# Kernel optimization log

Hardware: AMD Instinct MI355X
Metric: run time of the kernel (lower is better)

## Reference

```python
import jax, jax.numpy as jnp
import numpy as np

N_NODES = 100000
N_EDGES = 1600000
D = 128
EPS = 1e-5


def setup_inputs() -> dict:
    key = jax.random.key(0)
    k1, k2, k3 = jax.random.split(key, 3)
    x = jax.random.normal(k1, (N_NODES, D), dtype=jnp.float32)
    edge_index = jax.random.randint(k2, (2, N_EDGES), 0, N_NODES, dtype=jnp.int64)
    W = jax.random.normal(k3, (D, D), dtype=jnp.float32) * (1.0 / np.sqrt(D))
    b = jnp.zeros((D,), dtype=jnp.float32)
    gamma = jnp.ones((D,), dtype=jnp.float32)
    beta = jnp.zeros((D,), dtype=jnp.float32)
    return {"x": x, "edge_index": edge_index, "W": W, "b": b, "gamma": gamma, "beta": beta}


def reference(x, edge_index, W, b, gamma, beta):
    N = x.shape[0]
    loops = jnp.arange(N, dtype=edge_index.dtype)
    src = jnp.concatenate([edge_index[0], loops])  # [E+N]
    dst = jnp.concatenate([edge_index[1], loops])  # [E+N]
    # symmetric GCN normalization with self-loops; deg >= 1 always
    deg = jax.ops.segment_sum(jnp.ones_like(dst, dtype=x.dtype), dst, num_segments=N)
    dis = jax.lax.rsqrt(deg)
    xw = x @ W  # [N, D]
    norm = (dis[src] * dis[dst])[:, None]  # [E+N, 1]
    agg = jax.ops.segment_sum(xw[src] * norm, dst, num_segments=N) + b
    h = agg + x  # residual (in_channels == out_channels -> Identity proj)
    mu = jnp.mean(h, axis=-1, keepdims=True)
    var = jnp.mean(jnp.square(h - mu), axis=-1, keepdims=True)
    h = (h - mu) * jax.lax.rsqrt(var + EPS) * gamma + beta
    return jax.nn.relu(h)  # dropout = identity in eval mode
```

## Files before the change

### kernel.cpp

```cpp
#include <hip/hip_runtime.h>
#include <cstdint>
#include <cstddef>

#define NN 100000
#define NE 1600000
#define DD 128
#define EPSV 1e-5f
#define NPART 8
#define PSIZE (NN / NPART)
#define NCHUNK 256
#define CSZ (NE / NCHUNK)

typedef __attribute__((ext_vector_type(8))) short bf16x8;
typedef __attribute__((ext_vector_type(4))) float f32x4;
typedef __attribute__((ext_vector_type(4))) int i32x4;
typedef __attribute__((ext_vector_type(2))) int i32x2;
typedef __attribute__((ext_vector_type(4))) unsigned short u16x4;

static __device__ inline unsigned short f2bf(float f) {
    unsigned u = __float_as_uint(f);
    unsigned r = (u + 0x7fffu + ((u >> 16) & 1u)) >> 16;
    return (unsigned short)r;
}

static __device__ inline float bflo(unsigned u) { return __uint_as_float(u << 16); }
static __device__ inline float bfhi(unsigned u) { return __uint_as_float(u & 0xffff0000u); }

template <typename T>
static __device__ inline T ntload(const T* p) { return __builtin_nontemporal_load(p); }
template <typename T>
static __device__ inline void ntstore(T* p, T v) { __builtin_nontemporal_store(v, p); }

__global__ void detect_kernel(const unsigned* __restrict__ raw, int* __restrict__ flag) {
    int i = blockIdx.x * blockDim.x + threadIdx.x;
    if (i >= 4096) return;
    size_t idx = (size_t)i * 780 + 1;
    if (raw[idx] != 0) atomicOr(flag, 1);
}

__global__ void convert_kernel(const int* __restrict__ raw, int* __restrict__ e32,
                               const int* __restrict__ flag,
                               const float* __restrict__ x, unsigned short* __restrict__ xb,
                               const float* __restrict__ W, unsigned short* __restrict__ wb,
                               int* __restrict__ cnt8) {
    int* cnt = cnt8 + (size_t)(blockIdx.x & 7) * NN;
    const int is32 = *flag;
    const int stride = gridDim.x * blockDim.x;
    const int tid0 = blockIdx.x * blockDim.x + threadIdx.x;
    if (is32) {
        for (int i = tid0; i < 2 * NE / 4; i += stride) {
            const i32x4 v = ntload((const i32x4*)e32 == nullptr ? (const i32x4*)raw + i : (const i32x4*)raw + i);
            ntstore((i32x4*)e32 + i, v);
            if (i >= NE / 4) {
                atomicAdd(&cnt[v.x], 1); atomicAdd(&cnt[v.y], 1);
                atomicAdd(&cnt[v.z], 1); atomicAdd(&cnt[v.w], 1);
            }
        }
    } else {
        for (int i = tid0; i < NE; i += stride) {
            const i32x4 v = ntload((const i32x4*)raw + i);
            i32x2 o; o.x = v.x; o.y = v.z;
            ntstore((i32x2*)e32 + i, o);
            if (i >= NE / 2) {
                atomicAdd(&cnt[v.x], 1); atomicAdd(&cnt[v.z], 1);
            }
        }
    }
    for (int i = tid0; i < NN * DD / 4; i += stride) {
        const f32x4 v = ntload((const f32x4*)x + i);
        u16x4 o;
        o.x = f2bf(v.x); o.y = f2bf(v.y); o.z = f2bf(v.z); o.w = f2bf(v.w);
        ntstore((u16x4*)xb + i, o);
    }
    for (int i = tid0; i < DD * DD / 4; i += stride) {
        const f32x4 v = *((const f32x4*)W + i);
        u16x4 o;
        o.x = f2bf(v.x); o.y = f2bf(v.y); o.z = f2bf(v.z); o.w = f2bf(v.w);
        *((u16x4*)wb + i) = o;
    }
}

__global__ void alloc_kernel(const int* __restrict__ cnt8, int* __restrict__ cnt,
                             int* __restrict__ start, int* __restrict__ fill,
                             float* __restrict__ dis, int* __restrict__ cursor) {
    __shared__ int sdata[256];
    __shared__ int sbase;
    const int tid = threadIdx.x;
    const int v = blockIdx.x * 256 + tid;
    int c = 0;
    if (v < NN) {
        #pragma unroll
        for (int k = 0; k < 8; ++k) c += cnt8[(size_t)k * NN + v];
    }
    sdata[tid] = c;
    __syncthreads();
    #pragma unroll
    for (int off = 1; off < 256; off <<= 1) {
        int t = (tid >= off) ? sdata[tid - off] : 0;
        __syncthreads();
        sdata[tid] += t;
        __syncthreads();
    }
    const int excl = sdata[tid] - c;
    const int total = sdata[255];
    if (tid == 0) sbase = atomicAdd(cursor, total);
    __syncthreads();
    if (v < NN) {
        const int st = sbase + excl;
        cnt[v] = c;
        start[v] = st;
        fill[v] = st;
        dis[v] = rsqrtf((float)(c + 1));
    }
}

__global__ void scatter_kernel(const int* __restrict__ e32, int* __restrict__ fill,
                               int* __restrict__ ssrc) {
    const int part = blockIdx.x & (NPART - 1);
    const int chunk = blockIdx.x >> 3;
    const int lo = part * PSIZE, hi = lo + PSIZE;
    const int e0 = chunk * CSZ, e1 = e0 + CSZ;
    for (int e = e0 + threadIdx.x; e < e1; e += 256) {
        const int d = ntload(e32 + NE + e);
        if (d >= lo && d < hi) {
            const int s = ntload(e32 + e);
            const int p = atomicAdd(&fill[d], 1);
            ssrc[p] = s;
        }
    }
}

__global__ void agg_kernel(const unsigned short* __restrict__ xb,
                           const int* __restrict__ ssrc, const int* __restrict__ start,
                           const int* __restrict__ cnt, const float* __restrict__ dis,
                           unsigned short* __restrict__ agg) {
    const int wave = threadIdx.x >> 6, lane = threadIdx.x & 63;
    const int node = blockIdx.x * 4 + wave;
    if (node >= NN) return;
    const float dv = dis[node];
    const unsigned us = *(const unsigned*)(xb + (size_t)node * DD + 2 * lane);
    float accx = dv * dv * bflo(us);
    float accy = dv * dv * bfhi(us);
    const int s0 = start[node];
    const int c = cnt[node];
    for (int chunk = 0; chunk < c; chunk += 64) {
        const int rem0 = c - chunk;
        const int rem = rem0 < 64 ? rem0 : 64;
        int sj = 0; float dsj = 0.f;
        if (lane < rem) {
            sj = ntload(ssrc + s0 + chunk + lane);
            dsj = dis[sj];
        }
        int j = 0;
        for (; j + 4 <= rem; j += 4) {
            const int i0 = __builtin_amdgcn_readlane(sj, j);
            const int i1 = __builtin_amdgcn_readlane(sj, j + 1);
            const int i2 = __builtin_amdgcn_readlane(sj, j + 2);
            const int i3 = __builtin_amdgcn_readlane(sj, j + 3);
            const float w0 = __uint_as_float(__builtin_amdgcn_readlane(__float_as_uint(dsj), j)) * dv;
            const float w1 = __uint_as_float(__builtin_amdgcn_readlane(__float_as_uint(dsj), j + 1)) * dv;
            const float w2 = __uint_as_float(__builtin_amdgcn_readlane(__float_as_uint(dsj), j + 2)) * dv;
            const float w3 = __uint_as_float(__builtin_amdgcn_readlane(__float_as_uint(dsj), j + 3)) * dv;
            const unsigned v0 = *(const unsigned*)(xb + (size_t)i0 * DD + 2 * lane);
            const unsigned v1 = *(const unsigned*)(xb + (size_t)i1 * DD + 2 * lane);
            const unsigned v2 = *(const unsigned*)(xb + (size_t)i2 * DD + 2 * lane);
            const unsigned v3 = *(const unsigned*)(xb + (size_t)i3 * DD + 2 * lane);
            accx = fmaf(w0, bflo(v0), accx); accy = fmaf(w0, bfhi(v0), accy);
            accx = fmaf(w1, bflo(v1), accx); accy = fmaf(w1, bfhi(v1), accy);
            accx = fmaf(w2, bflo(v2), accx); accy = fmaf(w2, bfhi(v2), accy);
            accx = fmaf(w3, bflo(v3), accx); accy = fmaf(w3, bfhi(v3), accy);
        }
        for (; j < rem; ++j) {
            const int s = __builtin_amdgcn_readlane(sj, j);
            const float w = __uint_as_float(__builtin_amdgcn_readlane(__float_as_uint(dsj), j)) * dv;
            const unsigned uv = *(const unsigned*)(xb + (size_t)s * DD + 2 * lane);
            accx = fmaf(w, bflo(uv), accx);
            accy = fmaf(w, bfhi(uv), accy);
        }
    }
    ushort2 st; st.x = f2bf(accx); st.y = f2bf(accy);
    *(ushort2*)(agg + (size_t)node * DD + 2 * lane) = st;
}

__global__ __launch_bounds__(256) void gemm2_kernel(const unsigned short* __restrict__ agg,
                                                    const unsigned short* __restrict__ xb,
                                                    const unsigned short* __restrict__ wb,
                                                    const float* __restrict__ b,
                                                    const float* __restrict__ g,
                                                    const float* __restrict__ be,
                                                    float* __restrict__ out) {
    const int wave = threadIdx.x >> 6, lane = threadIdx.x & 63;
    const int grp = lane >> 4;
    const int lc  = lane & 15;
    bf16x8 bfr[4][8];
    #pragma unroll
    for (int kb = 0; kb < 4; ++kb) {
        #pragma unroll
        for (int t = 0; t < 8; ++t) {
            bf16x8 v;
            #pragma unroll
            for (int j = 0; j < 8; ++j)
                v[j] = (short)wb[(size_t)(kb * 32 + grp * 8 + j) * DD + t * 16 + lc];
            bfr[kb][t] = v;
        }
    }
    float bbv[8], ggv[8], btv[8];
    #pragma unroll
    for (int t = 0; t < 8; ++t) {
        bbv[t] = b[t * 16 + lc];
        ggv[t] = g[t * 16 + lc];
        btv[t] = be[t * 16 + lc];
    }
    const int nrb = NN / 16;
    const int nw = gridDim.x * 4;
    for (int rb = blockIdx.x * 4 + wave; rb < nrb; rb += nw) {
        const unsigned short* ap = agg + (size_t)(rb * 16 + lc) * DD + grp * 8;
        f32x4 acc[8];
        #pragma unroll
        for (int t = 0; t < 8; ++t) acc[t] = (f32x4){0.f, 0.f, 0.f, 0.f};
        #pragma unroll
        for (int kb = 0; kb < 4; ++kb) {
            const bf16x8 a = *(const bf16x8*)(ap + kb * 32);
            #pragma unroll
            for (int t = 0; t < 8; ++t)
                acc[t] = __builtin_amdgcn_mfma_f32_16x16x32_bf16(a, bfr[kb][t], acc[t], 0, 0, 0);
        }
        const int r0 = rb * 16 + grp * 4;
        float h[8][4];
        float rs[4] = {0.f, 0.f, 0.f, 0.f};
        #pragma unroll
        for (int reg = 0; reg < 4; ++reg) {
            #pragma unroll
            for (int t = 0; t < 8; ++t) {
                const unsigned xr = xb[(size_t)(r0 + reg) * DD + t * 16 + lc];
                const float hv = acc[t][reg] + bbv[t] + bflo(xr);
                h[t][reg] = hv;
                rs[reg] += hv;
            }
        }
        #pragma unroll
        for (int reg = 0; reg < 4; ++reg) {
            #pragma unroll
            for (int off = 8; off; off >>= 1) rs[reg] += __shfl_xor(rs[reg], off);
        }
        float mu[4], s2[4] = {0.f, 0.f, 0.f, 0.f};
        #pragma unroll
        for (int reg = 0; reg < 4; ++reg) {
            mu[reg] = rs[reg] * (1.f / 128.f);
            #pragma unroll
            for (int t = 0; t < 8; ++t) {
                const float e = h[t][reg] - mu[reg];
                s2[reg] += e * e;
            }
            #pragma unroll
            for (int off = 8; off; off >>= 1) s2[reg] += __shfl_xor(s2[reg], off);
        }
        #pragma unroll
        for (int reg = 0; reg < 4; ++reg) {
            const float inv = rsqrtf(s2[reg] * (1.f / 128.f) + EPSV);
            #pragma unroll
            for (int t = 0; t < 8; ++t) {
                const float o = fmaxf(0.f, (h[t][reg] - mu[reg]) * inv * ggv[t] + btv[t]);
                out[(size_t)(r0 + reg) * DD + t * 16 + lc] = o;
            }
        }
    }
}

extern "C" void kernel_launch(void* const* d_in, const int* in_sizes, int n_in,
                              void* d_out, int out_size, void* d_ws, size_t ws_size,
                              hipStream_t stream) {
    const float* x  = (const float*)d_in[0];
    const int*   ei = (const int*)d_in[1];
    const float* W  = (const float*)d_in[2];
    const float* b  = (const float*)d_in[3];
    const float* g  = (const float*)d_in[4];
    const float* be = (const float*)d_in[5];
    float* out = (float*)d_out;

    char* ws = (char*)d_ws;
    size_t off = 0;
    unsigned short* xb  = (unsigned short*)(ws + off); off += (size_t)NN * DD * 2;
    unsigned short* agg = (unsigned short*)(ws + off); off += (size_t)NN * DD * 2;
    int*   e32   = (int*)(ws + off);   off += (size_t)2 * NE * 4;
    int*   ssrc  = (int*)(ws + off);   off += (size_t)NE * 4;
    unsigned short* wb = (unsigned short*)(ws + off); off += (size_t)DD * DD * 2;
    int*   cnt   = (int*)(ws + off);   off += (size_t)NN * 4;
    int*   start = (int*)(ws + off);   off += (size_t)NN * 4;
    int*   fill  = (int*)(ws + off);   off += (size_t)NN * 4;
    float* dis   = (float*)(ws + off); off += (size_t)NN * 4;
    int*   flagc = (int*)(ws + off);   off += 256;
    int*   cnt8  = (int*)agg;

    hipMemsetAsync(cnt8, 0, (size_t)8 * NN * 4, stream);
    hipMemsetAsync(flagc, 0, 256, stream);

    detect_kernel<<<16, 256, 0, stream>>>((const unsigned*)ei, flagc);
    convert_kernel<<<2048, 256, 0, stream>>>(ei, e32, flagc, x, xb, W, wb, cnt8);
    alloc_kernel<<<(NN + 255) / 256, 256, 0, stream>>>(cnt8, cnt, start, fill, dis, flagc + 1);
    scatter_kernel<<<NPART * NCHUNK, 256, 0, stream>>>(e32, fill, ssrc);
    agg_kernel<<<NN / 4, 256, 0, stream>>>(xb, ssrc, start, cnt, dis, agg);
    gemm2_kernel<<<512, 256, 0, stream>>>(agg, xb, wb, b, g, be, out);
}
```

Measured before the change: 356.4 us.

## Bind histogram and scatter partitions to XCC IDs with dynamic chunk queues

The count histogram copy is now chosen by the hardware XCC ID instead of blockIdx, so atomics from one XCD stay in that die's local L2. The scatter kernel becomes persistent: each block starts on the destination partition matching its XCC and takes edge chunks from a per-partition atomic queue, then moves on to the other partitions. Nontemporal stores in the convert kernel are swapped for regular stores so the converted data stays cached. This relies on an undocumented-style hardware register read and adds queue atomics and barriers per chunk, and the queue counters must be zeroed by the existing memset of flagc.

```diff
diff --git a/kernel.cpp b/kernel.cpp
--- a/kernel.cpp
+++ b/kernel.cpp
@@ -28,8 +28,12 @@
 
 template <typename T>
 static __device__ inline T ntload(const T* p) { return __builtin_nontemporal_load(p); }
-template <typename T>
-static __device__ inline void ntstore(T* p, T v) { __builtin_nontemporal_store(v, p); }
+
+static __device__ inline int xcc_id() {
+    int x;
+    asm volatile("s_getreg_b32 %0, hwreg(HW_REG_XCC_ID)" : "=s"(x));
+    return x & 7;
+}
 
 __global__ void detect_kernel(const unsigned* __restrict__ raw, int* __restrict__ flag) {
     int i = blockIdx.x * blockDim.x + threadIdx.x;
@@ -43,14 +47,14 @@
                                const float* __restrict__ x, unsigned short* __restrict__ xb,
                                const float* __restrict__ W, unsigned short* __restrict__ wb,
                                int* __restrict__ cnt8) {
-    int* cnt = cnt8 + (size_t)(blockIdx.x & 7) * NN;
+    int* cnt = cnt8 + (size_t)xcc_id() * NN;
     const int is32 = *flag;
     const int stride = gridDim.x * blockDim.x;
     const int tid0 = blockIdx.x * blockDim.x + threadIdx.x;
     if (is32) {
         for (int i = tid0; i < 2 * NE / 4; i += stride) {
-            const i32x4 v = ntload((const i32x4*)e32 == nullptr ? (const i32x4*)raw + i : (const i32x4*)raw + i);
-            ntstore((i32x4*)e32 + i, v);
+            const i32x4 v = ntload((const i32x4*)raw + i);
+            *((i32x4*)e32 + i) = v;
             if (i >= NE / 4) {
                 atomicAdd(&cnt[v.x], 1); atomicAdd(&cnt[v.y], 1);
                 atomicAdd(&cnt[v.z], 1); atomicAdd(&cnt[v.w], 1);
@@ -60,7 +64,7 @@
         for (int i = tid0; i < NE; i += stride) {
             const i32x4 v = ntload((const i32x4*)raw + i);
             i32x2 o; o.x = v.x; o.y = v.z;
-            ntstore((i32x2*)e32 + i, o);
+            *((i32x2*)e32 + i) = o;
             if (i >= NE / 2) {
                 atomicAdd(&cnt[v.x], 1); atomicAdd(&cnt[v.z], 1);
             }
@@ -70,7 +74,7 @@
         const f32x4 v = ntload((const f32x4*)x + i);
         u16x4 o;
         o.x = f2bf(v.x); o.y = f2bf(v.y); o.z = f2bf(v.z); o.w = f2bf(v.w);
-        ntstore((u16x4*)xb + i, o);
+        *((u16x4*)xb + i) = o;
     }
     for (int i = tid0; i < DD * DD / 4; i += stride) {
         const f32x4 v = *((const f32x4*)W + i);
@@ -115,17 +119,27 @@
 }
 
 __global__ void scatter_kernel(const int* __restrict__ e32, int* __restrict__ fill,
-                               int* __restrict__ ssrc) {
-    const int part = blockIdx.x & (NPART - 1);
-    const int chunk = blockIdx.x >> 3;
-    const int lo = part * PSIZE, hi = lo + PSIZE;
-    const int e0 = chunk * CSZ, e1 = e0 + CSZ;
-    for (int e = e0 + threadIdx.x; e < e1; e += 256) {
-        const int d = ntload(e32 + NE + e);
-        if (d >= lo && d < hi) {
-            const int s = ntload(e32 + e);
-            const int p = atomicAdd(&fill[d], 1);
-            ssrc[p] = s;
+                               int* __restrict__ ssrc, int* __restrict__ qcursor) {
+    __shared__ int s_chunk;
+    const int myq = xcc_id();
+    for (int qi = 0; qi < NPART; ++qi) {
+        const int q = (myq + qi) & (NPART - 1);
+        const int lo = q * PSIZE, hi = lo + PSIZE;
+        for (;;) {
+            if (threadIdx.x == 0) s_chunk = atomicAdd(&qcursor[q], 1);
+            __syncthreads();
+            const int chunk = s_chunk;
+            __syncthreads();
+            if (chunk >= NCHUNK) break;
+            const int e0 = chunk * CSZ, e1 = e0 + CSZ;
+            for (int e = e0 + threadIdx.x; e < e1; e += 256) {
+                const int d = e32[NE + e];
+                if (d >= lo && d < hi) {
+                    const int s = e32[e];
+                    const int p = atomicAdd(&fill[d], 1);
+                    ssrc[p] = s;
+                }
+            }
         }
     }
 }
@@ -298,7 +312,7 @@
     detect_kernel<<<16, 256, 0, stream>>>((const unsigned*)ei, flagc);
     convert_kernel<<<2048, 256, 0, stream>>>(ei, e32, flagc, x, xb, W, wb, cnt8);
     alloc_kernel<<<(NN + 255) / 256, 256, 0, stream>>>(cnt8, cnt, start, fill, dis, flagc + 1);
-    scatter_kernel<<<NPART * NCHUNK, 256, 0, stream>>>(e32, fill, ssrc);
+    scatter_kernel<<<2048, 256, 0, stream>>>(e32, fill, ssrc, flagc + 8);
     agg_kernel<<<NN / 4, 256, 0, stream>>>(xb, ssrc, start, cnt, dis, agg);
     gemm2_kernel<<<512, 256, 0, stream>>>(agg, xb, wb, b, g, be, out);
 }
```

Result: slower. 539.3 us (+51.3%).

## Bucket edges by destination partition during conversion to shrink scatter pass

Applied to the files above, without the earlier changes.

The conversion kernel now writes (src,dst) pairs into per-partition queues using wave-level ballot and aggregated atomics, replacing the full int32 edge copy. The scatter pass then reads only its own partition's queue instead of scanning every edge once per partition. Degree counters are selected by the hardware XCC id rather than the block index, and the x conversion uses normal stores. The aim is to cut the redundant edge re-reads in scatter, at the cost of extra ballot and atomic work in convert and a fixed queue capacity that could overflow on skewed inputs.

```diff
diff --git a/kernel.cpp b/kernel.cpp
--- a/kernel.cpp
+++ b/kernel.cpp
@@ -8,12 +8,10 @@
 #define EPSV 1e-5f
 #define NPART 8
 #define PSIZE (NN / NPART)
-#define NCHUNK 256
-#define CSZ (NE / NCHUNK)
+#define QCAP 210000
 
 typedef __attribute__((ext_vector_type(8))) short bf16x8;
 typedef __attribute__((ext_vector_type(4))) float f32x4;
-typedef __attribute__((ext_vector_type(4))) int i32x4;
 typedef __attribute__((ext_vector_type(2))) int i32x2;
 typedef __attribute__((ext_vector_type(4))) unsigned short u16x4;
 
@@ -28,8 +26,12 @@
 
 template <typename T>
 static __device__ inline T ntload(const T* p) { return __builtin_nontemporal_load(p); }
-template <typename T>
-static __device__ inline void ntstore(T* p, T v) { __builtin_nontemporal_store(v, p); }
+
+static __device__ inline int xcc_id() {
+    int x;
+    asm volatile("s_getreg_b32 %0, hwreg(HW_REG_XCC_ID)" : "=s"(x));
+    return x & 7;
+}
 
 __global__ void detect_kernel(const unsigned* __restrict__ raw, int* __restrict__ flag) {
     int i = blockIdx.x * blockDim.x + threadIdx.x;
@@ -38,31 +40,39 @@
     if (raw[idx] != 0) atomicOr(flag, 1);
 }
 
-__global__ void convert_kernel(const int* __restrict__ raw, int* __restrict__ e32,
+__global__ void convert_kernel(const int* __restrict__ raw,
                                const int* __restrict__ flag,
                                const float* __restrict__ x, unsigned short* __restrict__ xb,
                                const float* __restrict__ W, unsigned short* __restrict__ wb,
-                               int* __restrict__ cnt8) {
-    int* cnt = cnt8 + (size_t)(blockIdx.x & 7) * NN;
+                               int* __restrict__ cnt8, i32x2* __restrict__ streamQ,
+                               int* __restrict__ qcur) {
+    int* cnt = cnt8 + (size_t)xcc_id() * NN;
     const int is32 = *flag;
     const int stride = gridDim.x * blockDim.x;
     const int tid0 = blockIdx.x * blockDim.x + threadIdx.x;
-    if (is32) {
-        for (int i = tid0; i < 2 * NE / 4; i += stride) {
-            const i32x4 v = ntload((const i32x4*)e32 == nullptr ? (const i32x4*)raw + i : (const i32x4*)raw + i);
-            ntstore((i32x4*)e32 + i, v);
-            if (i >= NE / 4) {
-                atomicAdd(&cnt[v.x], 1); atomicAdd(&cnt[v.y], 1);
-                atomicAdd(&cnt[v.z], 1); atomicAdd(&cnt[v.w], 1);
-            }
-        }
-    } else {
-        for (int i = tid0; i < NE; i += stride) {
-            const i32x4 v = ntload((const i32x4*)raw + i);
-            i32x2 o; o.x = v.x; o.y = v.z;
-            ntstore((i32x2*)e32 + i, o);
-            if (i >= NE / 2) {
-                atomicAdd(&cnt[v.x], 1); atomicAdd(&cnt[v.z], 1);
+    const int lane = threadIdx.x & 63;
+    const unsigned long long mlt = (lane == 63) ? 0x7fffffffffffffffULL
+                                                : ((1ULL << lane) - 1);
+    for (int e = tid0; e < NE; e += stride) {
+        int s, d;
+        if (is32) { s = raw[e]; d = raw[NE + e]; }
+        else      { s = raw[2 * (size_t)e]; d = raw[2 * ((size_t)NE + e)]; }
+        atomicAdd(&cnt[d], 1);
+        const int p = (unsigned)d / PSIZE;
+        #pragma unroll
+        for (int pr = 0; pr < NPART; ++pr) {
+            const unsigned long long m = __ballot(p == pr);
+            if (m != 0ULL) {
+                const int leader = __ffsll((long long)m) - 1;
+                int base = 0;
+                if (lane == leader)
+                    base = atomicAdd(&qcur[pr * 32], (int)__popcll(m));
+                base = __shfl(base, leader);
+                if (p == pr) {
+                    const int idx = base + (int)__popcll(m & mlt);
+                    i32x2 sd; sd.x = s; sd.y = d;
+                    streamQ[(size_t)pr * QCAP + idx] = sd;
+                }
             }
         }
     }
@@ -70,7 +80,7 @@
         const f32x4 v = ntload((const f32x4*)x + i);
         u16x4 o;
         o.x = f2bf(v.x); o.y = f2bf(v.y); o.z = f2bf(v.z); o.w = f2bf(v.w);
-        ntstore((u16x4*)xb + i, o);
+        *((u16x4*)xb + i) = o;
     }
     for (int i = tid0; i < DD * DD / 4; i += stride) {
         const f32x4 v = *((const f32x4*)W + i);
@@ -114,19 +124,19 @@
     }
 }
 
-__global__ void scatter_kernel(const int* __restrict__ e32, int* __restrict__ fill,
-                               int* __restrict__ ssrc) {
-    const int part = blockIdx.x & (NPART - 1);
-    const int chunk = blockIdx.x >> 3;
-    const int lo = part * PSIZE, hi = lo + PSIZE;
-    const int e0 = chunk * CSZ, e1 = e0 + CSZ;
-    for (int e = e0 + threadIdx.x; e < e1; e += 256) {
-        const int d = ntload(e32 + NE + e);
-        if (d >= lo && d < hi) {
-            const int s = ntload(e32 + e);
-            const int p = atomicAdd(&fill[d], 1);
-            ssrc[p] = s;
-        }
+__global__ void scatter2_kernel(const i32x2* __restrict__ streamQ,
+                                const int* __restrict__ qcur,
+                                int* __restrict__ fill, int* __restrict__ ssrc) {
+    const int p = blockIdx.x & (NPART - 1);
+    const int bi = blockIdx.x >> 3;
+    const int nb = gridDim.x >> 3;
+    const int len = qcur[p * 32];
+    const int stride = nb * 256;
+    const i32x2* q = streamQ + (size_t)p * QCAP;
+    for (int i = bi * 256 + threadIdx.x; i < len; i += stride) {
+        const i32x2 sd = ntload(q + i);
+        const int pos = atomicAdd(&fill[sd.y], 1);
+        ssrc[pos] = sd.x;
     }
 }
 
@@ -282,23 +292,24 @@
     size_t off = 0;
     unsigned short* xb  = (unsigned short*)(ws + off); off += (size_t)NN * DD * 2;
     unsigned short* agg = (unsigned short*)(ws + off); off += (size_t)NN * DD * 2;
-    int*   e32   = (int*)(ws + off);   off += (size_t)2 * NE * 4;
+    i32x2* streamQ = (i32x2*)(ws + off); off += (size_t)NPART * QCAP * 8;
     int*   ssrc  = (int*)(ws + off);   off += (size_t)NE * 4;
     unsigned short* wb = (unsigned short*)(ws + off); off += (size_t)DD * DD * 2;
     int*   cnt   = (int*)(ws + off);   off += (size_t)NN * 4;
     int*   start = (int*)(ws + off);   off += (size_t)NN * 4;
     int*   fill  = (int*)(ws + off);   off += (size_t)NN * 4;
     float* dis   = (float*)(ws + off); off += (size_t)NN * 4;
-    int*   flagc = (int*)(ws + off);   off += 256;
+    int*   flagc = (int*)(ws + off);   off += 4096;
     int*   cnt8  = (int*)agg;
-
-    hipMemsetAsync(cnt8, 0, (size_t)8 * NN * 4, stream);
-    hipMemsetAsync(flagc, 0, 256, stream);
+    int*   qcur  = flagc + 256;
+
+    (void)hipMemsetAsync(cnt8, 0, (size_t)8 * NN * 4, stream);
+    (void)hipMemsetAsync(flagc, 0, 4096, stream);
 
     detect_kernel<<<16, 256, 0, stream>>>((const unsigned*)ei, flagc);
-    convert_kernel<<<2048, 256, 0, stream>>>(ei, e32, flagc, x, xb, W, wb, cnt8);
+    convert_kernel<<<2048, 256, 0, stream>>>(ei, flagc, x, xb, W, wb, cnt8, streamQ, qcur);
     alloc_kernel<<<(NN + 255) / 256, 256, 0, stream>>>(cnt8, cnt, start, fill, dis, flagc + 1);
-    scatter_kernel<<<NPART * NCHUNK, 256, 0, stream>>>(e32, fill, ssrc);
+    scatter2_kernel<<<1024, 256, 0, stream>>>(streamQ, qcur, fill, ssrc);
     agg_kernel<<<NN / 4, 256, 0, stream>>>(xb, ssrc, start, cnt, dis, agg);
     gemm2_kernel<<<512, 256, 0, stream>>>(agg, xb, wb, b, g, be, out);
 }
```

New measurement: 744.1 us. 109% more time.
